# Kernel tuning notes

Hardware: AMD Instinct MI355X
Metric: run time of the kernel (lower is better)

## Reference

```python
import jax, jax.numpy as jnp
import numpy as np

E = 8      # num_experts
R = 32     # LoRA rank
D = 1024   # in_features (d_model)
H = 4096   # out_features of fc1 (hidden)
B = 2
S = 2048
SCALING = 1.0 / R  # lora_alpha / rank with alpha=1


def setup_inputs() -> dict:
    key = jax.random.key(0)
    ks = jax.random.split(key, 9)
    def w(k, shape, scale=0.02):
        return jax.random.normal(k, shape, dtype=jnp.float32) * scale
    return {
        "x": jax.random.normal(ks[0], (B, S, D), dtype=jnp.float32),
        "router_w": w(ks[1], (E, D)),
        "router_b": jnp.zeros((E,), jnp.float32),
        "fc1_w": w(ks[2], (H, D)),
        "fc1_b": jnp.zeros((H,), jnp.float32),
        "fc2_w": w(ks[3], (D, H)),
        "fc2_b": jnp.zeros((D,), jnp.float32),
        "A_down": w(ks[4], (E, R, D)),
        "Ab_down": jnp.zeros((E, R), jnp.float32),
        "B_down": w(ks[5], (E, H, R)),
        "Bb_down": jnp.zeros((E, H), jnp.float32),
        "A_up": w(ks[6], (E, R, H)),
        "Ab_up": jnp.zeros((E, R), jnp.float32),
        "B_up": w(ks[7], (E, D, R)),
        "Bb_up": jnp.zeros((E, D), jnp.float32),
    }


def _moe_lora(x, mask, A, Ab, Bw, Bb):
    # x: [B,S,din]; mask: one-hot [B,S,E]; A: [E,R,din]; Bw: [E,dout,R]
    # rank-stage for all experts is cheap (R=32), select per token via one-hot
    h = jnp.einsum('bsd,erd->bser', x, A) + Ab          # [B,S,E,R]
    hsel = jnp.einsum('bser,bse->bsr', h, mask)          # [B,S,R]
    out = jnp.zeros(x.shape[:2] + (Bw.shape[1],), dtype=x.dtype)
    for e in range(E):  # fixed small expert count; avoids [B,S,E,dout] blowup
        out = out + mask[..., e:e + 1] * (hsel @ Bw[e].T + Bb[e])
    return out * SCALING


def reference(x, router_w, router_b, fc1_w, fc1_b, fc2_w, fc2_b,
              A_down, Ab_down, B_down, Bb_down,
              A_up, Ab_up, B_up, Bb_up):
    logits = x @ router_w.T + router_b                   # [B,S,E]
    routing = jax.nn.softmax(logits, axis=-1)
    index = jnp.argmax(logits, axis=-1)                  # top-1 expert [B,S]
    mask = jax.nn.one_hot(index, E, dtype=x.dtype)       # y_hard [B,S,E]
    expert_choice = mask - jax.lax.stop_gradient(routing) + routing
    # down: frozen fc1 + sparse LoRA (dropout layers in eval mode -> identity)
    down = x @ fc1_w.T + fc1_b + _moe_lora(x, mask, A_down, Ab_down, B_down, Bb_down)
    a = jax.nn.gelu(down, approximate=False)             # F.gelu exact
    up = a @ fc2_w.T + fc2_b + _moe_lora(a, mask, A_up, Ab_up, B_up, Bb_up)
    return up, routing, expert_choice
```

## Files before the change

kernel.cpp:

```cpp
#include <hip/hip_runtime.h>
#include <hip/hip_bf16.h>
#include <math.h>
#include <stdint.h>

#define E_ 8
#define R_ 32
#define D_ 1024
#define H_ 4096
#define NTOK 4096
#define M_MAX 5120
#define TILES_MAX 40
#define SCALING 0.03125f

typedef __attribute__((ext_vector_type(8))) __bf16 bf16x8;
typedef __attribute__((ext_vector_type(8))) unsigned short ushort8;
typedef __attribute__((ext_vector_type(4))) float floatx4;

__device__ __forceinline__ unsigned short f2b(float f) {
    union { float f; unsigned int i; } v; v.f = f;
    unsigned int x = v.i;
    x += 0x7fffu + ((x >> 16) & 1u);
    return (unsigned short)(x >> 16);
}
__device__ __forceinline__ float gelu_fast(float v) {
    float u = v * (0.7978845608028654f + 0.0356774080857f * v * v);
    float t = __expf(-2.f * fabsf(u));
    float th = (1.f - t) * __builtin_amdgcn_rcpf(1.f + t);
    th = (u >= 0.f) ? th : -th;
    return 0.5f * v * (1.f + th);
}

#define GLOAD_LDS16(g, l) __builtin_amdgcn_global_load_lds( \
    (const __attribute__((address_space(1))) void*)(g),     \
    (__attribute__((address_space(3))) void*)(l), 16, 0, 0)

__global__ __launch_bounds__(256) void k_prep(
    const float* __restrict__ w1, const float* __restrict__ w2,
    const float* __restrict__ Ad, const float* __restrict__ Bd,
    const float* __restrict__ Au, const float* __restrict__ Bu,
    unsigned short* __restrict__ w1b, unsigned short* __restrict__ w2b,
    unsigned short* __restrict__ Adb, unsigned short* __restrict__ Bdb,
    unsigned short* __restrict__ Aub, unsigned short* __restrict__ Bub,
    const float* __restrict__ x, const float* __restrict__ rw,
    const float* __restrict__ rb,
    float* __restrict__ out, int* __restrict__ idx)
{
    if (blockIdx.x < 5376) {
        long g = ((long)blockIdx.x * 256 + threadIdx.x) * 8;
        const float* src; unsigned short* dst; long off;
        if      (g <  4194304L) { src = w1; dst = w1b; off = 0; }
        else if (g <  8388608L) { src = w2; dst = w2b; off = 4194304L; }
        else if (g <  8650752L) { src = Ad; dst = Adb; off = 8388608L; }
        else if (g <  9699328L) { src = Bd; dst = Bdb; off = 8650752L; }
        else if (g < 10747904L) { src = Au; dst = Aub; off = 9699328L; }
        else                    { src = Bu; dst = Bub; off = 10747904L; }
        long i = g - off;
        float4 a = *(const float4*)(src + i);
        float4 b = *(const float4*)(src + i + 4);
        ushort8 o;
        o[0] = f2b(a.x); o[1] = f2b(a.y); o[2] = f2b(a.z); o[3] = f2b(a.w);
        o[4] = f2b(b.x); o[5] = f2b(b.y); o[6] = f2b(b.z); o[7] = f2b(b.w);
        *(ushort8*)(dst + i) = o;
        return;
    }
    const int wave = threadIdx.x >> 6, lane = threadIdx.x & 63;
    const int t = (blockIdx.x - 5376) * 4 + wave;
    const float4* xr = (const float4*)(x + (size_t)t * D_);
    float4 xv[4];
#pragma unroll
    for (int s = 0; s < 4; ++s) xv[s] = xr[lane + 64 * s];
    float acc[E_];
#pragma unroll
    for (int e = 0; e < E_; ++e) {
        const float4* wr = (const float4*)(rw + (size_t)e * D_);
        float s = 0.f;
#pragma unroll
        for (int u = 0; u < 4; ++u) {
            float4 wv = wr[lane + 64 * u];
            s += xv[u].x * wv.x + xv[u].y * wv.y + xv[u].z * wv.z + xv[u].w * wv.w;
        }
        acc[e] = s;
    }
#pragma unroll
    for (int e = 0; e < E_; ++e) {
#pragma unroll
        for (int m = 32; m > 0; m >>= 1) acc[e] += __shfl_xor(acc[e], m, 64);
        acc[e] += rb[e];
    }
    int best = 0;
#pragma unroll
    for (int e = 1; e < E_; ++e) if (acc[e] > acc[best]) best = e;
    const float mx = acc[best];
    float pr[E_]; float se = 0.f;
#pragma unroll
    for (int e = 0; e < E_; ++e) { pr[e] = expf(acc[e] - mx); se += pr[e]; }
    const float inv = 1.f / se;
    if (lane < E_) {
        float r = pr[lane] * inv;
        out[(size_t)NTOK * D_ + (size_t)t * E_ + lane] = r;
        float maskv = (lane == best) ? 1.f : 0.f;
        out[(size_t)NTOK * D_ + (size_t)NTOK * E_ + (size_t)t * E_ + lane] = (maskv - r) + r;
    }
    if (lane == 0) idx[t] = best;
}

__global__ __launch_bounds__(256) void k_scan(
    const int* __restrict__ idx, int* __restrict__ hdr,
    int* __restrict__ tile_e, int* __restrict__ gather)
{
    __shared__ int cnt[256][E_];
    __shared__ int tot[E_], base[E_];
    const int tid = threadIdx.x;
    for (int m = tid; m < M_MAX; m += 256) gather[m] = -1;
    int c[E_];
#pragma unroll
    for (int e = 0; e < E_; ++e) c[e] = 0;
    for (int t = tid * 16; t < tid * 16 + 16; ++t) c[idx[t] & 7]++;
#pragma unroll
    for (int e = 0; e < E_; ++e) cnt[tid][e] = c[e];
    __syncthreads();
    if (tid < E_) {
        int run = 0;
        for (int i = 0; i < 256; ++i) { int v = cnt[i][tid]; cnt[i][tid] = run; run += v; }
        tot[tid] = run;
    }
    __syncthreads();
    if (tid == 0) {
        int b = 0, tp = 0;
        for (int e = 0; e < E_; ++e) {
            base[e] = b;
            int nt = (tot[e] + 127) >> 7;
            for (int k = 0; k < nt; ++k) tile_e[tp++] = e;
            b += nt << 7;
        }
        hdr[0] = b;
        hdr[1] = tp;
        for (int k = tp; k < TILES_MAX; ++k) tile_e[k] = 0;
    }
    __syncthreads();
    int p[E_];
#pragma unroll
    for (int e = 0; e < E_; ++e) p[e] = base[e] + cnt[tid][e];
    for (int t = tid * 16; t < tid * 16 + 16; ++t) { int e = idx[t] & 7; gather[p[e]++] = t; }
}

__global__ __launch_bounds__(128) void k_gather(
    const float* __restrict__ x, const int* __restrict__ gather,
    unsigned short* __restrict__ xg)
{
    const int m = blockIdx.x, tid = threadIdx.x;
    const int t = gather[m];
    ushort8* dst = (ushort8*)(xg + (size_t)m * D_);
    ushort8 o;
    if ((unsigned)t < (unsigned)NTOK) {
        const float4* src = (const float4*)(x + (size_t)t * D_);
        float4 a = src[tid * 2], b = src[tid * 2 + 1];
        o[0] = f2b(a.x); o[1] = f2b(a.y); o[2] = f2b(a.z); o[3] = f2b(a.w);
        o[4] = f2b(b.x); o[5] = f2b(b.y); o[6] = f2b(b.z); o[7] = f2b(b.w);
    } else {
        o = (ushort8)(0);
    }
    dst[tid] = o;
}

__global__ __launch_bounds__(256) void k_lora_a2(
    const unsigned short* __restrict__ A,
    const unsigned short* __restrict__ W,
    const float* __restrict__ Ab,
    const int* __restrict__ hdr, const int* __restrict__ tile_e,
    unsigned short* __restrict__ outb,
    int Ktot)
{
    const int mtile = blockIdx.y;
    int ntiles = hdr[1]; if (ntiles > TILES_MAX) ntiles = TILES_MAX;
    if (mtile >= ntiles) return;
    const int e = tile_e[mtile] & 7;
    const int m0 = mtile * 128 + blockIdx.x * 32;
    const int wave = threadIdx.x >> 6, lane = threadIdx.x & 63;
    const int q = lane >> 4, l16 = lane & 15;
    const int Ks = Ktot >> 2;
    const int kbase = wave * Ks;
    const floatx4 z4 = {0.f, 0.f, 0.f, 0.f};
    floatx4 acc[2][2] = {{z4, z4}, {z4, z4}};
    const bf16x8* A0 = (const bf16x8*)(A + (size_t)(m0 + l16) * Ktot);
    const bf16x8* A1 = (const bf16x8*)(A + (size_t)(m0 + 16 + l16) * Ktot);
    const bf16x8* W0 = (const bf16x8*)(W + ((size_t)e * 32 + l16) * Ktot);
    const bf16x8* W1 = (const bf16x8*)(W + ((size_t)e * 32 + 16 + l16) * Ktot);
    for (int k = kbase; k < kbase + Ks; k += 32) {
        int u = (k >> 3) + q;
        bf16x8 a0 = A0[u], a1 = A1[u];
        bf16x8 b0 = W0[u], b1 = W1[u];
        acc[0][0] = __builtin_amdgcn_mfma_f32_16x16x32_bf16(a0, b0, acc[0][0], 0, 0, 0);
        acc[0][1] = __builtin_amdgcn_mfma_f32_16x16x32_bf16(a0, b1, acc[0][1], 0, 0, 0);
        acc[1][0] = __builtin_amdgcn_mfma_f32_16x16x32_bf16(a1, b0, acc[1][0], 0, 0, 0);
        acc[1][1] = __builtin_amdgcn_mfma_f32_16x16x32_bf16(a1, b1, acc[1][1], 0, 0, 0);
    }
    __shared__ float red[4][32][32];
#pragma unroll
    for (int mi = 0; mi < 2; ++mi)
#pragma unroll
        for (int ni = 0; ni < 2; ++ni)
#pragma unroll
            for (int r = 0; r < 4; ++r)
                red[wave][mi * 16 + q * 4 + r][ni * 16 + l16] = acc[mi][ni][r];
    __syncthreads();
    for (int i = threadIdx.x; i < 1024; i += 256) {
        int lr = i >> 5, c = i & 31;
        float s = red[0][lr][c] + red[1][lr][c] + red[2][lr][c] + red[3][lr][c];
        outb[(size_t)(m0 + lr) * 32 + c] = f2b(SCALING * (s + Ab[e * 32 + c]));
    }
}

template <int KTOT, bool IS_FC1, int NSPLIT>
__global__ __launch_bounds__(256) void k_mlp(
    const unsigned short* __restrict__ Amat,
    const unsigned short* __restrict__ Wmat,
    const float* __restrict__ bias,
    const unsigned short* __restrict__ lora_h,
    const unsigned short* __restrict__ lora_B,
    const float* __restrict__ lora_b,
    const int* __restrict__ hdr, const int* __restrict__ tile_e,
    const int* __restrict__ gather,
    unsigned short* __restrict__ outb,
    float* __restrict__ outf,
    float* __restrict__ P,
    int NOUT)
{
    const int mtile = blockIdx.y;
    int ntiles = hdr[1]; if (ntiles > TILES_MAX) ntiles = TILES_MAX;
    if (mtile >= ntiles) return;
    const int e = tile_e[mtile] & 7;
    const int h0 = blockIdx.x * 128;
    const int m0 = mtile * 128;
    const bool extras = (NSPLIT == 1) || (blockIdx.z == 0);
    const int Kslice = KTOT / NSPLIT;
    const int kstart = blockIdx.z * Kslice;
    __shared__ bf16x8 As[1024];
    __shared__ bf16x8 Bs[1024];
    const int tid = threadIdx.x;
    const int lane = tid & 63;
    const int q = lane >> 4, l16 = lane & 15;
    const int wave = tid >> 6;
    const int wm = wave & 1, wn = wave >> 1;
    const floatx4 z4 = {0.f, 0.f, 0.f, 0.f};
    floatx4 acc[4][4];
#pragma unroll
    for (int mi = 0; mi < 4; ++mi)
#pragma unroll
        for (int ni = 0; ni < 4; ++ni) acc[mi][ni] = z4;

    const unsigned short* Abase = Amat + (size_t)m0 * KTOT;
    const unsigned short* Bbase = Wmat + (size_t)h0 * KTOT;

    for (int k0 = kstart; k0 < kstart + Kslice; k0 += 64) {
#pragma unroll
        for (int rnd = 0; rnd < 4; ++rnd) {
            int s = rnd * 256 + tid;
            int row = s >> 3;
            int jj = (s & 7) ^ (row & 7);
            const unsigned short* ga = Abase + (size_t)row * KTOT + k0 + jj * 8;
            const unsigned short* gb = Bbase + (size_t)row * KTOT + k0 + jj * 8;
            GLOAD_LDS16(ga, As + rnd * 256 + wave * 64);
            GLOAD_LDS16(gb, Bs + rnd * 256 + wave * 64);
        }
        __syncthreads();
#pragma unroll
        for (int ka = 0; ka < 2; ++ka) {
            bf16x8 af[4], bfr[4];
#pragma unroll
            for (int mi = 0; mi < 4; ++mi) {
                int row = wm * 64 + mi * 16 + l16;
                af[mi] = As[row * 8 + ((ka * 4 + q) ^ (row & 7))];
            }
#pragma unroll
            for (int ni = 0; ni < 4; ++ni) {
                int row = wn * 64 + ni * 16 + l16;
                bfr[ni] = Bs[row * 8 + ((ka * 4 + q) ^ (row & 7))];
            }
#pragma unroll
            for (int mi = 0; mi < 4; ++mi)
#pragma unroll
                for (int ni = 0; ni < 4; ++ni)
                    acc[mi][ni] = __builtin_amdgcn_mfma_f32_16x16x32_bf16(af[mi], bfr[ni], acc[mi][ni], 0, 0, 0);
        }
        __syncthreads();
    }

    if (extras) {
        bf16x8 a2[4], b2[4];
#pragma unroll
        for (int mi = 0; mi < 4; ++mi)
            a2[mi] = *(const bf16x8*)(lora_h + (size_t)(m0 + wm * 64 + mi * 16 + l16) * 32 + q * 8);
#pragma unroll
        for (int ni = 0; ni < 4; ++ni)
            b2[ni] = *(const bf16x8*)(lora_B + ((size_t)e * NOUT + h0 + wn * 64 + ni * 16 + l16) * 32 + q * 8);
#pragma unroll
        for (int mi = 0; mi < 4; ++mi)
#pragma unroll
            for (int ni = 0; ni < 4; ++ni)
                acc[mi][ni] = __builtin_amdgcn_mfma_f32_16x16x32_bf16(a2[mi], b2[ni], acc[mi][ni], 0, 0, 0);
    }

#pragma unroll
    for (int ni = 0; ni < 4; ++ni) {
        int gh = h0 + wn * 64 + ni * 16 + l16;
        float bv = extras ? (bias[gh] + SCALING * lora_b[e * NOUT + gh]) : 0.f;
#pragma unroll
        for (int mi = 0; mi < 4; ++mi) {
#pragma unroll
            for (int r = 0; r < 4; ++r) {
                int gm = m0 + wm * 64 + mi * 16 + q * 4 + r;
                float v = acc[mi][ni][r] + bv;
                if (IS_FC1) {
                    outb[(size_t)gm * NOUT + gh] = f2b(gelu_fast(v));
                } else if (extras) {
                    int t = gather[gm];
                    if ((unsigned)t < (unsigned)NTOK) outf[(size_t)t * NOUT + gh] = v;
                } else {
                    P[(size_t)gm * NOUT + gh] = v;
                }
            }
        }
    }
}

__global__ __launch_bounds__(256) void k_reduce(
    const float* __restrict__ P, const int* __restrict__ gather,
    float* __restrict__ out)
{
    const int m = blockIdx.x;
    const int t = gather[m];
    if ((unsigned)t >= (unsigned)NTOK) return;
    const float4* p4 = (const float4*)(P + (size_t)m * D_);
    float4* o4 = (float4*)(out + (size_t)t * D_);
    int i = threadIdx.x;
    float4 a = o4[i], b = p4[i];
    a.x += b.x; a.y += b.y; a.z += b.z; a.w += b.w;
    o4[i] = a;
}

#define OFF_IDX      0u
#define OFF_HDR      16384u
#define OFF_TILE     16640u
#define OFF_GATHER   16896u
#define OFF_XG       37376u
#define OFF_W1B      10523136u
#define OFF_ADB      18911744u
#define OFF_BDB      19436032u
#define OFF_HSB      21533184u
#define OFF_P        37376u
#define OFF_AG       21860864u
#define OFF_HUB      63803904u
#define OFF_W2B      64131584u
#define OFF_AUB      72520192u
#define OFF_BUB      74617344u
#define WS_NEEDED    75141632u

extern "C" void kernel_launch(void* const* d_in, const int* in_sizes, int n_in,
                              void* d_out, int out_size, void* d_ws, size_t ws_size,
                              hipStream_t stream)
{
    (void)out_size;
    if (ws_size < (size_t)WS_NEEDED) return;
    if (n_in < 15 || in_sizes[0] != NTOK * D_ || in_sizes[3] != H_ * D_ ||
        in_sizes[5] != D_ * H_ || in_sizes[9] != E_ * H_ * R_) return;

    const float* x   = (const float*)d_in[0];
    const float* rw  = (const float*)d_in[1];
    const float* rb  = (const float*)d_in[2];
    const float* w1  = (const float*)d_in[3];
    const float* b1  = (const float*)d_in[4];
    const float* w2  = (const float*)d_in[5];
    const float* b2  = (const float*)d_in[6];
    const float* Ad  = (const float*)d_in[7];
    const float* Abd = (const float*)d_in[8];
    const float* Bd  = (const float*)d_in[9];
    const float* Bbd = (const float*)d_in[10];
    const float* Au  = (const float*)d_in[11];
    const float* Abu = (const float*)d_in[12];
    const float* Bu  = (const float*)d_in[13];
    const float* Bbu = (const float*)d_in[14];
    float* out = (float*)d_out;
    char* ws = (char*)d_ws;

    int* idx            = (int*)(ws + OFF_IDX);
    int* hdr            = (int*)(ws + OFF_HDR);
    int* tile_e         = (int*)(ws + OFF_TILE);
    int* gather         = (int*)(ws + OFF_GATHER);
    unsigned short* xg  = (unsigned short*)(ws + OFF_XG);
    unsigned short* hsb = (unsigned short*)(ws + OFF_HSB);
    unsigned short* ag  = (unsigned short*)(ws + OFF_AG);
    unsigned short* hub = (unsigned short*)(ws + OFF_HUB);
    unsigned short* w1b = (unsigned short*)(ws + OFF_W1B);
    unsigned short* w2b = (unsigned short*)(ws + OFF_W2B);
    unsigned short* Adb = (unsigned short*)(ws + OFF_ADB);
    unsigned short* Bdb = (unsigned short*)(ws + OFF_BDB);
    unsigned short* Aub = (unsigned short*)(ws + OFF_AUB);
    unsigned short* Bub = (unsigned short*)(ws + OFF_BUB);
    float* P            = (float*)(ws + OFF_P);

    k_prep<<<6400, 256, 0, stream>>>(w1, w2, Ad, Bd, Au, Bu,
                                     w1b, w2b, Adb, Bdb, Aub, Bub,
                                     x, rw, rb, out, idx);
    k_scan<<<1, 256, 0, stream>>>(idx, hdr, tile_e, gather);
    k_gather<<<M_MAX, 128, 0, stream>>>(x, gather, xg);
    k_lora_a2<<<dim3(4, TILES_MAX), 256, 0, stream>>>(xg, Adb, Abd, hdr, tile_e, hsb, D_);
    k_mlp<D_, true, 1><<<dim3(H_ / 128, TILES_MAX, 1), 256, 0, stream>>>(
        xg, w1b, b1, hsb, Bdb, Bbd, hdr, tile_e, gather, ag, nullptr, nullptr, H_);
    k_lora_a2<<<dim3(4, TILES_MAX), 256, 0, stream>>>(ag, Aub, Abu, hdr, tile_e, hub, H_);
    k_mlp<H_, false, 2><<<dim3(D_ / 128, TILES_MAX, 2), 256, 0, stream>>>(
        ag, w2b, b2, hub, Bub, Bbu, hdr, tile_e, gather, nullptr, out, P, D_);
    k_reduce<<<M_MAX, 256, 0, stream>>>(P, gather, out);
}
```

Before: 309.1 us.

## Rewrite grouped MLP GEMM as 256x128 tile with triple-buffered LDS pipeline

Replaces the 128x128 single-buffered GEMM kernel with a 512-thread, 256x128-tile kernel. It uses a three-slot LDS ring with loads issued two k-steps ahead, split half-stage prefetches, s_setprio around the MFMA bursts and explicit vmcnt waits. The fc2 split-K path and its separate reduce kernel are dropped, so fc2 now runs unsplit with fewer blocks (8x20). The aim is to hide global-load latency and raise reuse per block, at the cost of fewer blocks for the fc2 GEMM and larger LDS use.

```diff
diff --git a/kernel.cpp b/kernel.cpp
--- a/kernel.cpp
+++ b/kernel.cpp
@@ -211,8 +211,19 @@
     }
 }
 
-template <int KTOT, bool IS_FC1, int NSPLIT>
-__global__ __launch_bounds__(256) void k_mlp(
+#define STG_H0(S2, KO) do { \
+    GLOAD_LDS16(Ar + (KO),                         As3 + (S2) * 2048 +        wave * 64); \
+    GLOAD_LDS16(Ar + (size_t)64  * KTOT + (KO),    As3 + (S2) * 2048 +  512 + wave * 64); \
+    GLOAD_LDS16(Br + (KO),                         Bs3 + (S2) * 1024 +        wave * 64); \
+} while (0)
+#define STG_H1(S2, KO) do { \
+    GLOAD_LDS16(Ar + (size_t)128 * KTOT + (KO),    As3 + (S2) * 2048 + 1024 + wave * 64); \
+    GLOAD_LDS16(Ar + (size_t)192 * KTOT + (KO),    As3 + (S2) * 2048 + 1536 + wave * 64); \
+    GLOAD_LDS16(Br + (size_t)64  * KTOT + (KO),    Bs3 + (S2) * 1024 +  512 + wave * 64); \
+} while (0)
+
+template <int KTOT, bool IS_FC1>
+__global__ __launch_bounds__(512, 2) void k_mlp8(
     const unsigned short* __restrict__ Amat,
     const unsigned short* __restrict__ Wmat,
     const float* __restrict__ bias,
@@ -223,25 +234,33 @@
     const int* __restrict__ gather,
     unsigned short* __restrict__ outb,
     float* __restrict__ outf,
-    float* __restrict__ P,
     int NOUT)
 {
-    const int mtile = blockIdx.y;
-    int ntiles = hdr[1]; if (ntiles > TILES_MAX) ntiles = TILES_MAX;
-    if (mtile >= ntiles) return;
-    const int e = tile_e[mtile] & 7;
+    constexpr int NT = KTOT / 64;
+    const int mt2 = blockIdx.y;
+    int nt128 = hdr[1]; if (nt128 > TILES_MAX) nt128 = TILES_MAX;
+    const int n256 = (nt128 + 1) >> 1;
+    if (mt2 >= n256) return;
+    const int m0 = mt2 * 256;
     const int h0 = blockIdx.x * 128;
-    const int m0 = mtile * 128;
-    const bool extras = (NSPLIT == 1) || (blockIdx.z == 0);
-    const int Kslice = KTOT / NSPLIT;
-    const int kstart = blockIdx.z * Kslice;
-    __shared__ bf16x8 As[1024];
-    __shared__ bf16x8 Bs[1024];
-    const int tid = threadIdx.x;
-    const int lane = tid & 63;
-    const int q = lane >> 4, l16 = lane & 15;
-    const int wave = tid >> 6;
-    const int wm = wave & 1, wn = wave >> 1;
+
+    __shared__ bf16x8 As3[6144];
+    __shared__ bf16x8 Bs3[3072];
+
+    const int tid  = threadIdx.x;
+    const int wave = tid >> 6, lane = tid & 63;
+    const int l16 = lane & 15, q = lane >> 4;
+    const int wm = wave & 3, wn = wave >> 2;
+    const int idx0 = q ^ (l16 & 7);
+    const int arow = wm * 64 + l16;
+    const int brow = wn * 64 + l16;
+    const int rrow = tid >> 3;
+    const int jj8  = (((tid & 7) ^ (rrow & 7)) << 3);
+    const unsigned short* Abase = Amat + (size_t)m0 * KTOT;
+    const unsigned short* Bbase = Wmat + (size_t)h0 * KTOT;
+    const unsigned short* Ar = Abase + (size_t)rrow * KTOT + jj8;
+    const unsigned short* Br = Bbase + (size_t)rrow * KTOT + jj8;
+
     const floatx4 z4 = {0.f, 0.f, 0.f, 0.f};
     floatx4 acc[4][4];
 #pragma unroll
@@ -249,94 +268,90 @@
 #pragma unroll
         for (int ni = 0; ni < 4; ++ni) acc[mi][ni] = z4;
 
-    const unsigned short* Abase = Amat + (size_t)m0 * KTOT;
-    const unsigned short* Bbase = Wmat + (size_t)h0 * KTOT;
-
-    for (int k0 = kstart; k0 < kstart + Kslice; k0 += 64) {
-#pragma unroll
-        for (int rnd = 0; rnd < 4; ++rnd) {
-            int s = rnd * 256 + tid;
-            int row = s >> 3;
-            int jj = (s & 7) ^ (row & 7);
-            const unsigned short* ga = Abase + (size_t)row * KTOT + k0 + jj * 8;
-            const unsigned short* gb = Bbase + (size_t)row * KTOT + k0 + jj * 8;
-            GLOAD_LDS16(ga, As + rnd * 256 + wave * 64);
-            GLOAD_LDS16(gb, Bs + rnd * 256 + wave * 64);
+    STG_H0(0, 0);  STG_H1(0, 0);
+    STG_H0(1, 64); STG_H1(1, 64);
+    asm volatile("s_waitcnt vmcnt(6)" ::: "memory");
+    __builtin_amdgcn_s_barrier();
+
+    int slot = 0, slot2 = 2;
+#pragma unroll 1
+    for (int kt = 0; kt < NT; ++kt) {
+        const int sA = slot << 11, sB = slot << 10;
+        const int ko2 = (kt + 2) << 6;
+        const bool more = (kt + 2) < NT;
+        bf16x8 af[4], bfr[4];
+#pragma unroll
+        for (int mi = 0; mi < 4; ++mi) af[mi]  = As3[sA + ((arow + mi * 16) << 3) + idx0];
+#pragma unroll
+        for (int ni = 0; ni < 4; ++ni) bfr[ni] = Bs3[sB + ((brow + ni * 16) << 3) + idx0];
+        if (more) STG_H0(slot2, ko2);
+        __builtin_amdgcn_s_barrier();
+        asm volatile("s_waitcnt lgkmcnt(0)" ::: "memory");
+        __builtin_amdgcn_s_setprio(1);
+#pragma unroll
+        for (int mi = 0; mi < 4; ++mi)
+#pragma unroll
+            for (int ni = 0; ni < 4; ++ni)
+                acc[mi][ni] = __builtin_amdgcn_mfma_f32_16x16x32_bf16(af[mi], bfr[ni], acc[mi][ni], 0, 0, 0);
+        __builtin_amdgcn_s_setprio(0);
+        __builtin_amdgcn_s_barrier();
+#pragma unroll
+        for (int mi = 0; mi < 4; ++mi) af[mi]  = As3[sA + ((arow + mi * 16) << 3) + (idx0 ^ 4)];
+#pragma unroll
+        for (int ni = 0; ni < 4; ++ni) bfr[ni] = Bs3[sB + ((brow + ni * 16) << 3) + (idx0 ^ 4)];
+        if (more) {
+            STG_H1(slot2, ko2);
+            asm volatile("s_waitcnt vmcnt(6)" ::: "memory");
+        } else {
+            asm volatile("s_waitcnt vmcnt(0)" ::: "memory");
         }
-        __syncthreads();
-#pragma unroll
-        for (int ka = 0; ka < 2; ++ka) {
-            bf16x8 af[4], bfr[4];
-#pragma unroll
-            for (int mi = 0; mi < 4; ++mi) {
-                int row = wm * 64 + mi * 16 + l16;
-                af[mi] = As[row * 8 + ((ka * 4 + q) ^ (row & 7))];
-            }
-#pragma unroll
-            for (int ni = 0; ni < 4; ++ni) {
-                int row = wn * 64 + ni * 16 + l16;
-                bfr[ni] = Bs[row * 8 + ((ka * 4 + q) ^ (row & 7))];
-            }
-#pragma unroll
-            for (int mi = 0; mi < 4; ++mi)
-#pragma unroll
-                for (int ni = 0; ni < 4; ++ni)
-                    acc[mi][ni] = __builtin_amdgcn_mfma_f32_16x16x32_bf16(af[mi], bfr[ni], acc[mi][ni], 0, 0, 0);
-        }
-        __syncthreads();
-    }
-
-    if (extras) {
-        bf16x8 a2[4], b2[4];
+        __builtin_amdgcn_s_barrier();
+        asm volatile("s_waitcnt lgkmcnt(0)" ::: "memory");
+        __builtin_amdgcn_s_setprio(1);
 #pragma unroll
         for (int mi = 0; mi < 4; ++mi)
-            a2[mi] = *(const bf16x8*)(lora_h + (size_t)(m0 + wm * 64 + mi * 16 + l16) * 32 + q * 8);
+#pragma unroll
+            for (int ni = 0; ni < 4; ++ni)
+                acc[mi][ni] = __builtin_amdgcn_mfma_f32_16x16x32_bf16(af[mi], bfr[ni], acc[mi][ni], 0, 0, 0);
+        __builtin_amdgcn_s_setprio(0);
+        __builtin_amdgcn_s_barrier();
+        slot  = (slot  == 2) ? 0 : slot  + 1;
+        slot2 = (slot2 == 2) ? 0 : slot2 + 1;
+    }
+
+    const int e = tile_e[(mt2 << 1) + (wm >> 1)] & 7;
+    bf16x8 a2[4], b2[4];
+#pragma unroll
+    for (int mi = 0; mi < 4; ++mi)
+        a2[mi] = *(const bf16x8*)(lora_h + (size_t)(m0 + wm * 64 + mi * 16 + l16) * 32 + q * 8);
+#pragma unroll
+    for (int ni = 0; ni < 4; ++ni)
+        b2[ni] = *(const bf16x8*)(lora_B + ((size_t)e * NOUT + h0 + wn * 64 + ni * 16 + l16) * 32 + q * 8);
+#pragma unroll
+    for (int mi = 0; mi < 4; ++mi)
 #pragma unroll
         for (int ni = 0; ni < 4; ++ni)
-            b2[ni] = *(const bf16x8*)(lora_B + ((size_t)e * NOUT + h0 + wn * 64 + ni * 16 + l16) * 32 + q * 8);
-#pragma unroll
-        for (int mi = 0; mi < 4; ++mi)
-#pragma unroll
-            for (int ni = 0; ni < 4; ++ni)
-                acc[mi][ni] = __builtin_amdgcn_mfma_f32_16x16x32_bf16(a2[mi], b2[ni], acc[mi][ni], 0, 0, 0);
-    }
+            acc[mi][ni] = __builtin_amdgcn_mfma_f32_16x16x32_bf16(a2[mi], b2[ni], acc[mi][ni], 0, 0, 0);
 
 #pragma unroll
     for (int ni = 0; ni < 4; ++ni) {
-        int gh = h0 + wn * 64 + ni * 16 + l16;
-        float bv = extras ? (bias[gh] + SCALING * lora_b[e * NOUT + gh]) : 0.f;
+        const int gh = h0 + wn * 64 + ni * 16 + l16;
+        const float bv = bias[gh] + SCALING * lora_b[e * NOUT + gh];
 #pragma unroll
         for (int mi = 0; mi < 4; ++mi) {
 #pragma unroll
             for (int r = 0; r < 4; ++r) {
-                int gm = m0 + wm * 64 + mi * 16 + q * 4 + r;
-                float v = acc[mi][ni][r] + bv;
+                const int gm = m0 + wm * 64 + mi * 16 + q * 4 + r;
+                const float v = acc[mi][ni][r] + bv;
                 if (IS_FC1) {
                     outb[(size_t)gm * NOUT + gh] = f2b(gelu_fast(v));
-                } else if (extras) {
-                    int t = gather[gm];
+                } else {
+                    const int t = gather[gm];
                     if ((unsigned)t < (unsigned)NTOK) outf[(size_t)t * NOUT + gh] = v;
-                } else {
-                    P[(size_t)gm * NOUT + gh] = v;
                 }
             }
         }
     }
-}
-
-__global__ __launch_bounds__(256) void k_reduce(
-    const float* __restrict__ P, const int* __restrict__ gather,
-    float* __restrict__ out)
-{
-    const int m = blockIdx.x;
-    const int t = gather[m];
-    if ((unsigned)t >= (unsigned)NTOK) return;
-    const float4* p4 = (const float4*)(P + (size_t)m * D_);
-    float4* o4 = (float4*)(out + (size_t)t * D_);
-    int i = threadIdx.x;
-    float4 a = o4[i], b = p4[i];
-    a.x += b.x; a.y += b.y; a.z += b.z; a.w += b.w;
-    o4[i] = a;
 }
 
 #define OFF_IDX      0u
@@ -348,7 +363,6 @@
 #define OFF_ADB      18911744u
 #define OFF_BDB      19436032u
 #define OFF_HSB      21533184u
-#define OFF_P        37376u
 #define OFF_AG       21860864u
 #define OFF_HUB      63803904u
 #define OFF_W2B      64131584u
@@ -397,7 +411,6 @@
     unsigned short* Bdb = (unsigned short*)(ws + OFF_BDB);
     unsigned short* Aub = (unsigned short*)(ws + OFF_AUB);
     unsigned short* Bub = (unsigned short*)(ws + OFF_BUB);
-    float* P            = (float*)(ws + OFF_P);
 
     k_prep<<<6400, 256, 0, stream>>>(w1, w2, Ad, Bd, Au, Bu,
                                      w1b, w2b, Adb, Bdb, Aub, Bub,
@@ -405,10 +418,9 @@
     k_scan<<<1, 256, 0, stream>>>(idx, hdr, tile_e, gather);
     k_gather<<<M_MAX, 128, 0, stream>>>(x, gather, xg);
     k_lora_a2<<<dim3(4, TILES_MAX), 256, 0, stream>>>(xg, Adb, Abd, hdr, tile_e, hsb, D_);
-    k_mlp<D_, true, 1><<<dim3(H_ / 128, TILES_MAX, 1), 256, 0, stream>>>(
-        xg, w1b, b1, hsb, Bdb, Bbd, hdr, tile_e, gather, ag, nullptr, nullptr, H_);
+    k_mlp8<D_, true><<<dim3(H_ / 128, TILES_MAX / 2), 512, 0, stream>>>(
+        xg, w1b, b1, hsb, Bdb, Bbd, hdr, tile_e, gather, ag, nullptr, H_);
     k_lora_a2<<<dim3(4, TILES_MAX), 256, 0, stream>>>(ag, Aub, Abu, hdr, tile_e, hub, H_);
-    k_mlp<H_, false, 2><<<dim3(D_ / 128, TILES_MAX, 2), 256, 0, stream>>>(
-        ag, w2b, b2, hub, Bub, Bbu, hdr, tile_e, gather, nullptr, out, P, D_);
-    k_reduce<<<M_MAX, 256, 0, stream>>>(P, gather, out);
-}
+    k_mlp8<H_, false><<<dim3(D_ / 128, TILES_MAX / 2), 512, 0, stream>>>(
+        ag, w2b, b2, hub, Bub, Bbu, hdr, tile_e, gather, nullptr, out, D_);
+}
```

New measurement: 301.9 us. 1.02x faster.

## Rewrite MLP GEMMs with multi-stage LDS ring pipeline and larger tiles

Applied to the files above, without the earlier changes.

Replaces the single-buffered 128x128 MLP GEMM with a templated kernel that keeps a 4–6 slot LDS ring of async global-to-LDS loads, using vmcnt waits and bare barriers so loads overlap MFMA work. Tiles grow to 256x256 (512 threads) for fc1 and 128x256 for fc2, and s_setprio is raised around the MFMA block. Block IDs are remapped so consecutive launches spread across XCD groups for cache locality. It trades much higher LDS and register use (32 accumulators per lane) for fewer loads per FLOP, and the 256-row fc1 tiles span two expert tiles, each wave half picking its own expert.

```diff
diff --git a/kernel.cpp b/kernel.cpp
--- a/kernel.cpp
+++ b/kernel.cpp
@@ -33,6 +33,13 @@
 #define GLOAD_LDS16(g, l) __builtin_amdgcn_global_load_lds( \
     (const __attribute__((address_space(1))) void*)(g),     \
     (__attribute__((address_space(3))) void*)(l), 16, 0, 0)
+
+template <int N> __device__ __forceinline__ void waitcnt_vm() {
+    static_assert(N == 0 || N == 8 || N == 24, "unsupported vmcnt");
+    if constexpr (N == 0)       asm volatile("s_waitcnt vmcnt(0)" ::: "memory");
+    else if constexpr (N == 8)  asm volatile("s_waitcnt vmcnt(8)" ::: "memory");
+    else if constexpr (N == 24) asm volatile("s_waitcnt vmcnt(24)" ::: "memory");
+}
 
 __global__ __launch_bounds__(256) void k_prep(
     const float* __restrict__ w1, const float* __restrict__ w2,
@@ -211,8 +218,8 @@
     }
 }
 
-template <int KTOT, bool IS_FC1, int NSPLIT>
-__global__ __launch_bounds__(256) void k_mlp(
+template <int KTOT, int BM, int NOUTC, bool IS_FC1, int NSPLIT>
+__global__ __launch_bounds__(BM * 2) void k_mlp9(
     const unsigned short* __restrict__ Amat,
     const unsigned short* __restrict__ Wmat,
     const float* __restrict__ bias,
@@ -223,79 +230,129 @@
     const int* __restrict__ gather,
     unsigned short* __restrict__ outb,
     float* __restrict__ outf,
-    float* __restrict__ P,
-    int NOUT)
-{
-    const int mtile = blockIdx.y;
-    int ntiles = hdr[1]; if (ntiles > TILES_MAX) ntiles = TILES_MAX;
-    if (mtile >= ntiles) return;
-    const int e = tile_e[mtile] & 7;
-    const int h0 = blockIdx.x * 128;
-    const int m0 = mtile * 128;
+    float* __restrict__ P)
+{
+    constexpr int T     = BM * 2;
+    constexpr int NX    = NOUTC / 256;
+    constexpr int RING  = (BM == 256) ? 4 : 6;
+    constexpr int NH    = (KTOT / NSPLIT) / 32;
+    constexpr int LA    = (BM * 4) / T;
+    constexpr int LB    = 1024 / T;
+    constexpr int LTOT  = LA + LB;
+    constexpr int VMST  = (RING - 2) * LTOT;
+    constexpr int ASLOT = BM * 32;
+    constexpr int BSLOT = 256 * 32;
+
+    __shared__ unsigned short As[RING * ASLOT];
+    __shared__ unsigned short Bs[RING * BSLOT];
+
+    int nt = hdr[1]; if (nt > TILES_MAX) nt = TILES_MAX;
+    const int ny = (BM == 256) ? ((nt + 1) >> 1) : nt;
+    const int nact = NX * ny;
+    const int lid = blockIdx.x + NX * blockIdx.y;
+    if (lid >= nact) return;
+    const int xc = lid & 7, jb = lid >> 3;
+    const int qd = nact >> 3, rmn = nact & 7;
+    const int tlin = xc * qd + (xc < rmn ? xc : rmn) + jb;
+    const int ty = tlin / NX, tx = tlin - ty * NX;
+    const int m0 = ty * BM, h0 = tx * 256;
+    const int kstart = (int)blockIdx.z * (KTOT / NSPLIT);
+
+    const int tid  = threadIdx.x;
+    const int wave = tid >> 6, lane = tid & 63;
+    const int l16 = lane & 15, q = lane >> 4;
+    const int wm = (BM == 256) ? (wave & 1) : 0;
+    const int wn = (BM == 256) ? (wave >> 1) : wave;
+
+    const unsigned short* Abase = Amat + (size_t)m0 * KTOT + kstart;
+    const unsigned short* Bbase = Wmat + (size_t)h0 * KTOT + kstart;
+    const unsigned short* srcA[LA];
+    const unsigned short* srcB[LB];
+#pragma unroll
+    for (int la = 0; la < LA; ++la) {
+        int ci = tid + T * la, row = ci >> 2, j = ci & 3;
+        srcA[la] = Abase + (size_t)row * KTOT + ((j ^ ((row >> 2) & 3)) << 3);
+    }
+#pragma unroll
+    for (int lb = 0; lb < LB; ++lb) {
+        int ci = tid + T * lb, row = ci >> 2, j = ci & 3;
+        srcB[lb] = Bbase + (size_t)row * KTOT + ((j ^ ((row >> 2) & 3)) << 3);
+    }
+    auto stage = [&](int s) {
+#pragma unroll
+        for (int la = 0; la < LA; ++la) {
+            GLOAD_LDS16(srcA[la], As + s * ASLOT + (wave * 64 + T * la) * 8);
+            srcA[la] += 32;
+        }
+#pragma unroll
+        for (int lb = 0; lb < LB; ++lb) {
+            GLOAD_LDS16(srcB[lb], Bs + s * BSLOT + (wave * 64 + T * lb) * 8);
+            srcB[lb] += 32;
+        }
+    };
+
+    int aoff[8], boff[4];
+#pragma unroll
+    for (int mi = 0; mi < 8; ++mi) {
+        int row = wm * 128 + mi * 16 + l16;
+        aoff[mi] = row * 32 + ((q ^ ((row >> 2) & 3)) << 3);
+    }
+#pragma unroll
+    for (int ni = 0; ni < 4; ++ni) {
+        int row = wn * 64 + ni * 16 + l16;
+        boff[ni] = row * 32 + ((q ^ ((row >> 2) & 3)) << 3);
+    }
+
+    const floatx4 z4 = {0.f, 0.f, 0.f, 0.f};
+    floatx4 acc[8][4];
+#pragma unroll
+    for (int mi = 0; mi < 8; ++mi)
+#pragma unroll
+        for (int ni = 0; ni < 4; ++ni) acc[mi][ni] = z4;
+
+#pragma unroll
+    for (int h = 0; h < RING - 1; ++h) stage(h);
+    waitcnt_vm<VMST>();
+    __builtin_amdgcn_s_barrier();
+
+    int slot = 0, sstage = RING - 1;
+#pragma unroll 1
+    for (int h = 0; h < NH; ++h) {
+        bf16x8 af[8], bfr[4];
+        const unsigned short* Abuf = As + slot * ASLOT;
+        const unsigned short* Bbuf = Bs + slot * BSLOT;
+#pragma unroll
+        for (int mi = 0; mi < 8; ++mi) af[mi]  = *(const bf16x8*)(Abuf + aoff[mi]);
+#pragma unroll
+        for (int ni = 0; ni < 4; ++ni) bfr[ni] = *(const bf16x8*)(Bbuf + boff[ni]);
+        const bool more = h < NH - (RING - 1);
+        if (more) stage(sstage);
+        __builtin_amdgcn_s_setprio(1);
+#pragma unroll
+        for (int mi = 0; mi < 8; ++mi)
+#pragma unroll
+            for (int ni = 0; ni < 4; ++ni)
+                acc[mi][ni] = __builtin_amdgcn_mfma_f32_16x16x32_bf16(af[mi], bfr[ni], acc[mi][ni], 0, 0, 0);
+        __builtin_amdgcn_s_setprio(0);
+        if (more) waitcnt_vm<VMST>();
+        else      waitcnt_vm<0>();
+        __builtin_amdgcn_s_barrier();
+        slot   = (slot   + 1 == RING) ? 0 : slot   + 1;
+        sstage = (sstage + 1 == RING) ? 0 : sstage + 1;
+    }
+
     const bool extras = (NSPLIT == 1) || (blockIdx.z == 0);
-    const int Kslice = KTOT / NSPLIT;
-    const int kstart = blockIdx.z * Kslice;
-    __shared__ bf16x8 As[1024];
-    __shared__ bf16x8 Bs[1024];
-    const int tid = threadIdx.x;
-    const int lane = tid & 63;
-    const int q = lane >> 4, l16 = lane & 15;
-    const int wave = tid >> 6;
-    const int wm = wave & 1, wn = wave >> 1;
-    const floatx4 z4 = {0.f, 0.f, 0.f, 0.f};
-    floatx4 acc[4][4];
-#pragma unroll
-    for (int mi = 0; mi < 4; ++mi)
-#pragma unroll
-        for (int ni = 0; ni < 4; ++ni) acc[mi][ni] = z4;
-
-    const unsigned short* Abase = Amat + (size_t)m0 * KTOT;
-    const unsigned short* Bbase = Wmat + (size_t)h0 * KTOT;
-
-    for (int k0 = kstart; k0 < kstart + Kslice; k0 += 64) {
-#pragma unroll
-        for (int rnd = 0; rnd < 4; ++rnd) {
-            int s = rnd * 256 + tid;
-            int row = s >> 3;
-            int jj = (s & 7) ^ (row & 7);
-            const unsigned short* ga = Abase + (size_t)row * KTOT + k0 + jj * 8;
-            const unsigned short* gb = Bbase + (size_t)row * KTOT + k0 + jj * 8;
-            GLOAD_LDS16(ga, As + rnd * 256 + wave * 64);
-            GLOAD_LDS16(gb, Bs + rnd * 256 + wave * 64);
-        }
-        __syncthreads();
-#pragma unroll
-        for (int ka = 0; ka < 2; ++ka) {
-            bf16x8 af[4], bfr[4];
-#pragma unroll
-            for (int mi = 0; mi < 4; ++mi) {
-                int row = wm * 64 + mi * 16 + l16;
-                af[mi] = As[row * 8 + ((ka * 4 + q) ^ (row & 7))];
-            }
-#pragma unroll
-            for (int ni = 0; ni < 4; ++ni) {
-                int row = wn * 64 + ni * 16 + l16;
-                bfr[ni] = Bs[row * 8 + ((ka * 4 + q) ^ (row & 7))];
-            }
-#pragma unroll
-            for (int mi = 0; mi < 4; ++mi)
-#pragma unroll
-                for (int ni = 0; ni < 4; ++ni)
-                    acc[mi][ni] = __builtin_amdgcn_mfma_f32_16x16x32_bf16(af[mi], bfr[ni], acc[mi][ni], 0, 0, 0);
-        }
-        __syncthreads();
-    }
-
+    const int e = tile_e[ty * (BM / 128) + wm] & 7;
     if (extras) {
-        bf16x8 a2[4], b2[4];
-#pragma unroll
-        for (int mi = 0; mi < 4; ++mi)
-            a2[mi] = *(const bf16x8*)(lora_h + (size_t)(m0 + wm * 64 + mi * 16 + l16) * 32 + q * 8);
+        bf16x8 a2[8], b2[4];
+#pragma unroll
+        for (int mi = 0; mi < 8; ++mi)
+            a2[mi] = *(const bf16x8*)(lora_h + (size_t)(m0 + wm * 128 + mi * 16 + l16) * 32 + q * 8);
 #pragma unroll
         for (int ni = 0; ni < 4; ++ni)
-            b2[ni] = *(const bf16x8*)(lora_B + ((size_t)e * NOUT + h0 + wn * 64 + ni * 16 + l16) * 32 + q * 8);
-#pragma unroll
-        for (int mi = 0; mi < 4; ++mi)
+            b2[ni] = *(const bf16x8*)(lora_B + ((size_t)e * NOUTC + h0 + wn * 64 + ni * 16 + l16) * 32 + q * 8);
+#pragma unroll
+        for (int mi = 0; mi < 8; ++mi)
 #pragma unroll
             for (int ni = 0; ni < 4; ++ni)
                 acc[mi][ni] = __builtin_amdgcn_mfma_f32_16x16x32_bf16(a2[mi], b2[ni], acc[mi][ni], 0, 0, 0);
@@ -303,21 +360,22 @@
 
 #pragma unroll
     for (int ni = 0; ni < 4; ++ni) {
-        int gh = h0 + wn * 64 + ni * 16 + l16;
-        float bv = extras ? (bias[gh] + SCALING * lora_b[e * NOUT + gh]) : 0.f;
-#pragma unroll
-        for (int mi = 0; mi < 4; ++mi) {
+        const int gh = h0 + wn * 64 + ni * 16 + l16;
+        const float bv = extras ? (bias[gh] + SCALING * lora_b[e * NOUTC + gh]) : 0.f;
+#pragma unroll
+        for (int mi = 0; mi < 8; ++mi) {
+            const int gmb = m0 + wm * 128 + mi * 16 + q * 4;
 #pragma unroll
             for (int r = 0; r < 4; ++r) {
-                int gm = m0 + wm * 64 + mi * 16 + q * 4 + r;
-                float v = acc[mi][ni][r] + bv;
+                const int gm = gmb + r;
+                const float v = acc[mi][ni][r] + bv;
                 if (IS_FC1) {
-                    outb[(size_t)gm * NOUT + gh] = f2b(gelu_fast(v));
+                    outb[(size_t)gm * NOUTC + gh] = f2b(gelu_fast(v));
                 } else if (extras) {
-                    int t = gather[gm];
-                    if ((unsigned)t < (unsigned)NTOK) outf[(size_t)t * NOUT + gh] = v;
+                    const int t = gather[gm];
+                    if ((unsigned)t < (unsigned)NTOK) outf[(size_t)t * NOUTC + gh] = v;
                 } else {
-                    P[(size_t)gm * NOUT + gh] = v;
+                    P[(size_t)gm * NOUTC + gh] = v;
                 }
             }
         }
@@ -405,10 +463,10 @@
     k_scan<<<1, 256, 0, stream>>>(idx, hdr, tile_e, gather);
     k_gather<<<M_MAX, 128, 0, stream>>>(x, gather, xg);
     k_lora_a2<<<dim3(4, TILES_MAX), 256, 0, stream>>>(xg, Adb, Abd, hdr, tile_e, hsb, D_);
-    k_mlp<D_, true, 1><<<dim3(H_ / 128, TILES_MAX, 1), 256, 0, stream>>>(
-        xg, w1b, b1, hsb, Bdb, Bbd, hdr, tile_e, gather, ag, nullptr, nullptr, H_);
+    k_mlp9<D_, 256, H_, true, 1><<<dim3(16, 20, 1), 512, 0, stream>>>(
+        xg, w1b, b1, hsb, Bdb, Bbd, hdr, tile_e, gather, ag, nullptr, nullptr);
     k_lora_a2<<<dim3(4, TILES_MAX), 256, 0, stream>>>(ag, Aub, Abu, hdr, tile_e, hub, H_);
-    k_mlp<H_, false, 2><<<dim3(D_ / 128, TILES_MAX, 2), 256, 0, stream>>>(
-        ag, w2b, b2, hub, Bub, Bbu, hdr, tile_e, gather, nullptr, out, P, D_);
+    k_mlp9<H_, 128, D_, false, 2><<<dim3(4, 40, 2), 256, 0, stream>>>(
+        ag, w2b, b2, hub, Bub, Bbu, hdr, tile_e, gather, nullptr, out, P);
     k_reduce<<<M_MAX, 256, 0, stream>>>(P, gather, out);
 }
```

Measured after the change: 339.6 us. +9.9%, slower.
